# Kernel tuning notes

Hardware: AMD Instinct MI355X
Metric: run time of the kernel (lower is better)

## Reference

```python
import jax, jax.numpy as jnp
import numpy as np


def pool_windows(a, k):
    # a: [..., H, W] with k == stride (non-overlapping windows)
    lead = a.shape[:-2]
    H, W = a.shape[-2], a.shape[-1]
    a = a.reshape(*lead, H // k, k, W // k, k)
    a = jnp.moveaxis(a, -3, -2)            # [..., Ho, Wo, k, k]
    return a.reshape(*lead, H // k, W // k, k * k)


def setup_inputs() -> dict:
    key = jax.random.key(0)
    k1, k2 = jax.random.split(key)
    S, C, H, W = 258, 64, 64, 64
    x = jax.random.normal(k1, (S, C, H, W), dtype=jnp.float32)
    # noise layer (last row) is nonnegative by convention
    x = x.at[-1].set(jnp.abs(x[-1]))
    x_true = jax.random.normal(k2, (C, H, W), dtype=jnp.float32)
    return {"x": x, "x_true": x_true, "kernel_size": 2, "stride": 2}


def reference(x, x_true, kernel_size, stride):
    # Zonotope/interval abstract transformer for MaxPool2d.
    # x: [S, C, H, W]; row 0 = center, rows 1:-1 = eps coeffs, row -1 = noise.
    assert kernel_size == stride
    k = kernel_size

    # Interval bounds per element (sum-of-abs reduction over symbol layers)
    eps_abs = jnp.sum(jnp.abs(x[1:]), axis=0)           # [C, H, W]
    lo = x[0] - eps_abs
    hi = x[0] + eps_abs

    xw = pool_windows(x, k)                              # [S, C, Ho, Wo, K]
    lw = pool_windows(lo, k)                             # [C, Ho, Wo, K]
    uw = pool_windows(hi, k)
    K = xw.shape[-1]

    # Candidate: window element with the largest lower bound
    i_star = jnp.argmax(lw, axis=-1)                     # [C, Ho, Wo]
    l_star = jnp.take_along_axis(lw, i_star[..., None], axis=-1)[..., 0]
    u_max = jnp.max(uw, axis=-1)

    # Max upper bound among the other window elements
    oh = jnp.arange(K) == i_star[..., None]              # one-hot of i_star
    u_other = jnp.max(jnp.where(oh, -jnp.inf, uw), axis=-1)

    # Exact case: the candidate dominates every other element -> pass its
    # affine form through. Otherwise fall back to the sound interval box
    # [l_star, u_max] (center +/- half-width in the noise layer).
    exact = l_star >= u_other                            # [C, Ho, Wo]

    gathered = jnp.take_along_axis(
        xw, i_star[None, ..., None], axis=-1)[..., 0]    # [S, C, Ho, Wo]

    box_center = 0.5 * (l_star + u_max)
    box_noise = 0.5 * (u_max - l_star)

    out_center = jnp.where(exact, gathered[0], box_center)
    out_eps = jnp.where(exact[None], gathered[1:-1], 0.0)
    out_noise = jnp.where(exact, jnp.abs(gathered[-1]), box_noise)

    x_out = jnp.concatenate(
        [out_center[None], out_eps, out_noise[None]], axis=0)

    out_abs = jnp.sum(jnp.abs(x_out[1:]), axis=0)
    x_min = x_out[0] - out_abs
    x_max = x_out[0] + out_abs

    x_true_out = jnp.max(pool_windows(x_true, k), axis=-1)
    return x_out, x_min, x_max, x_true_out
```

## Files before the change

kernel.cpp:

```cpp
#include <hip/hip_runtime.h>
#include <math.h>

#define S    258
#define C    64
#define H    64
#define W    64
#define NP   65536
#define L    262144
#define XOUT (S * NP)
#define NSC  8
#define NQ   4

__global__ __launch_bounds__(256) void k_partial(const float* __restrict__ x,
                                                 float* __restrict__ part,
                                                 float* __restrict__ out) {
    const int b  = blockIdx.x;
    const int sc = b >> 8;
    const int c  = (b >> 2) & 63;
    const int q  = b & 3;
    const int t  = threadIdx.x;

    {
        float4 z = make_float4(0.f, 0.f, 0.f, 0.f);
        float4* zp = (float4*)(out + NP) + (size_t)b * 2048 + t;
        #pragma unroll
        for (int i = 0; i < 8; ++i) zp[i * 256] = z;
    }

    const int s0 = 1 + ((257 * sc) >> 3);
    const int s1 = 1 + ((257 * (sc + 1)) >> 3);

    const int base = c * (H * W) + q * 1024 + 4 * t;
    const float* px = x + (size_t)s0 * L + base;
    float4 acc = make_float4(0.f, 0.f, 0.f, 0.f);
    #pragma unroll 4
    for (int s = s0; s < s1; ++s) {
        float4 v = *(const float4*)px;
        acc.x += fabsf(v.x); acc.y += fabsf(v.y);
        acc.z += fabsf(v.z); acc.w += fabsf(v.w);
        px += L;
    }
    *(float4*)(part + (size_t)sc * L + c * (H * W) + q * 1024 + 4 * t) = acc;
}

__global__ __launch_bounds__(256) void k_decide(const float* __restrict__ x,
                                                const float* __restrict__ x_true,
                                                const float* __restrict__ part,
                                                float* __restrict__ out) {
    __shared__ int ex_n;
    __shared__ int ex_p[256];
    __shared__ int ex_pos[256];

    const int b = blockIdx.x;
    const int c = b >> 2;
    const int q = b & 3;
    const int t = threadIdx.x;
    if (t == 0) ex_n = 0;
    __syncthreads();

    const int r  = t >> 5;
    const int wo = t & 31;
    const int qbase   = c * (H * W) + q * 1024;
    const int loc_top = (2 * r) * W + 2 * wo;
    const int loc_bot = loc_top + W;

    float e0 = 0.f, e1 = 0.f, e2 = 0.f, e3 = 0.f;
    #pragma unroll
    for (int sc = 0; sc < NSC; ++sc) {
        const float* pp = part + (size_t)sc * L + qbase;
        float2 a = *(const float2*)(pp + loc_top);
        float2 d = *(const float2*)(pp + loc_bot);
        e0 += a.x; e1 += a.y; e2 += d.x; e3 += d.y;
    }

    float2 r0 = *(const float2*)(x + qbase + loc_top);
    float2 r1 = *(const float2*)(x + qbase + loc_bot);
    float x0[4]  = { r0.x, r0.y, r1.x, r1.y };
    float eps[4] = { e0, e1, e2, e3 };
    float lo[4], hi[4];
    #pragma unroll
    for (int e = 0; e < 4; ++e) { lo[e] = x0[e] - eps[e]; hi[e] = x0[e] + eps[e]; }

    int istar = 0;
    #pragma unroll
    for (int e = 1; e < 4; ++e) if (lo[e] > lo[istar]) istar = e;

    const float lstar = lo[istar];
    const float umax  = fmaxf(fmaxf(hi[0], hi[1]), fmaxf(hi[2], hi[3]));
    float uoth = -INFINITY;
    #pragma unroll
    for (int e = 0; e < 4; ++e) if (e != istar) uoth = fmaxf(uoth, hi[e]);

    const bool exact = (lstar >= uoth);
    const int  pos   = qbase + loc_top + (istar & 1) + (istar >> 1) * W;

    float center, noise;
    if (exact) {
        center = x0[istar];
        noise  = fabsf(x[(size_t)(S - 1) * L + pos]);
        int i  = atomicAdd(&ex_n, 1);
        ex_p[i]   = c * 1024 + q * 256 + t;
        ex_pos[i] = pos;
    } else {
        center = 0.5f * (lstar + umax);
        noise  = 0.5f * (umax - lstar);
    }

    const int p = c * 1024 + q * 256 + t;
    out[p] = center;
    out[(size_t)(S - 1) * NP + p] = noise;
    out[XOUT + p] = lstar;
    out[XOUT + NP + p] = umax;

    float2 t0 = *(const float2*)(x_true + qbase + loc_top);
    float2 t1 = *(const float2*)(x_true + qbase + loc_bot);
    out[XOUT + 2 * NP + p] = fmaxf(fmaxf(t0.x, t0.y), fmaxf(t1.x, t1.y));

    __syncthreads();
    const int n = ex_n;
    for (int j = 0; j < n; ++j) {
        out[(size_t)(1 + t) * NP + ex_p[j]] = x[(size_t)(1 + t) * L + ex_pos[j]];
    }
}

extern "C" void kernel_launch(void* const* d_in, const int* in_sizes, int n_in,
                              void* d_out, int out_size, void* d_ws, size_t ws_size,
                              hipStream_t stream) {
    const float* x      = (const float*)d_in[0];
    const float* x_true = (const float*)d_in[1];
    float* out  = (float*)d_out;
    float* part = (float*)d_ws;

    k_partial<<<NSC * C * NQ, 256, 0, stream>>>(x, part, out);
    k_decide<<<C * NQ, 256, 0, stream>>>(x, x_true, part, out);
}
```

Before: 383.5 us.

## Fuse partial abs-sum and window decision into a single kernel

```diff
diff --git a/kernel.cpp b/kernel.cpp
--- a/kernel.cpp
+++ b/kernel.cpp
@@ -3,118 +3,107 @@
 
 #define S    258
 #define C    64
-#define H    64
-#define W    64
+#define L    262144
 #define NP   65536
-#define L    262144
 #define XOUT (S * NP)
-#define NSC  8
-#define NQ   4
 
-__global__ __launch_bounds__(256) void k_partial(const float* __restrict__ x,
-                                                 float* __restrict__ part,
-                                                 float* __restrict__ out) {
+__global__ __launch_bounds__(256) void k_fused(const float* __restrict__ x,
+                                               const float* __restrict__ x_true,
+                                               float* __restrict__ out) {
+    __shared__ int ex_n;
+    __shared__ int ex_p[128];
+    __shared__ int ex_pos[128];
+
     const int b  = blockIdx.x;
-    const int sc = b >> 8;
-    const int c  = (b >> 2) & 63;
-    const int q  = b & 3;
+    const int c  = b >> 3;
+    const int hq = b & 7;
     const int t  = threadIdx.x;
+    if (t == 0) ex_n = 0;
 
     {
-        float4 z = make_float4(0.f, 0.f, 0.f, 0.f);
-        float4* zp = (float4*)(out + NP) + (size_t)b * 2048 + t;
+        const float4 z = make_float4(0.f, 0.f, 0.f, 0.f);
+        float4* o4 = (float4*)out + (size_t)(c * 256 + hq * 32 + (t & 31));
+        const int s0 = 1 + (t >> 5);
         #pragma unroll
-        for (int i = 0; i < 8; ++i) zp[i * 256] = z;
+        for (int i = 0; i < 32; ++i)
+            o4[(size_t)(s0 + i * 8) * 16384] = z;
     }
 
-    const int s0 = 1 + ((257 * sc) >> 3);
-    const int s1 = 1 + ((257 * (sc + 1)) >> 3);
+    const int slice = c * 4096 + hq * 512;
+    const float* px = x + slice + 2 * t;
 
-    const int base = c * (H * W) + q * 1024 + 4 * t;
-    const float* px = x + (size_t)s0 * L + base;
-    float4 acc = make_float4(0.f, 0.f, 0.f, 0.f);
-    #pragma unroll 4
-    for (int s = s0; s < s1; ++s) {
-        float4 v = *(const float4*)px;
-        acc.x += fabsf(v.x); acc.y += fabsf(v.y);
-        acc.z += fabsf(v.z); acc.w += fabsf(v.w);
-        px += L;
+    const float2 x0 = *(const float2*)px;
+    float e0 = 0.f, e1 = 0.f;
+    const float* ps = px + L;
+    #pragma unroll 8
+    for (int s = 1; s <= 256; ++s) {
+        float2 v = *(const float2*)ps;
+        e0 += fabsf(v.x);
+        e1 += fabsf(v.y);
+        ps += L;
     }
-    *(float4*)(part + (size_t)sc * L + c * (H * W) + q * 1024 + 4 * t) = acc;
-}
+    const float2 nz = *(const float2*)ps;
+    const float n0 = fabsf(nz.x), n1 = fabsf(nz.y);
+    e0 += n0;
+    e1 += n1;
 
-__global__ __launch_bounds__(256) void k_decide(const float* __restrict__ x,
-                                                const float* __restrict__ x_true,
-                                                const float* __restrict__ part,
-                                                float* __restrict__ out) {
-    __shared__ int ex_n;
-    __shared__ int ex_p[256];
-    __shared__ int ex_pos[256];
-
-    const int b = blockIdx.x;
-    const int c = b >> 2;
-    const int q = b & 3;
-    const int t = threadIdx.x;
-    if (t == 0) ex_n = 0;
     __syncthreads();
 
-    const int r  = t >> 5;
-    const int wo = t & 31;
-    const int qbase   = c * (H * W) + q * 1024;
-    const int loc_top = (2 * r) * W + 2 * wo;
-    const int loc_bot = loc_top + W;
+    const float ox0 = __shfl_xor(x0.x, 32, 64);
+    const float ox1 = __shfl_xor(x0.y, 32, 64);
+    const float oe0 = __shfl_xor(e0,   32, 64);
+    const float oe1 = __shfl_xor(e1,   32, 64);
+    const float on0 = __shfl_xor(n0,   32, 64);
+    const float on1 = __shfl_xor(n1,   32, 64);
 
-    float e0 = 0.f, e1 = 0.f, e2 = 0.f, e3 = 0.f;
-    #pragma unroll
-    for (int sc = 0; sc < NSC; ++sc) {
-        const float* pp = part + (size_t)sc * L + qbase;
-        float2 a = *(const float2*)(pp + loc_top);
-        float2 d = *(const float2*)(pp + loc_bot);
-        e0 += a.x; e1 += a.y; e2 += d.x; e3 += d.y;
+    const int lane = t & 63;
+    if (lane < 32) {
+        const float xc[4] = { x0.x, x0.y, ox0, ox1 };
+        const float ee[4] = { e0,   e1,   oe0, oe1 };
+        const float nn[4] = { n0,   n1,   on0, on1 };
+        float lo[4], hi[4];
+        #pragma unroll
+        for (int e = 0; e < 4; ++e) {
+            lo[e] = xc[e] - ee[e];
+            hi[e] = xc[e] + ee[e];
+        }
+
+        int istar = 0;
+        #pragma unroll
+        for (int e = 1; e < 4; ++e) if (lo[e] > lo[istar]) istar = e;
+
+        const float lstar = lo[istar];
+        const float umax  = fmaxf(fmaxf(hi[0], hi[1]), fmaxf(hi[2], hi[3]));
+        float uoth = -INFINITY;
+        #pragma unroll
+        for (int e = 0; e < 4; ++e) if (e != istar) uoth = fmaxf(uoth, hi[e]);
+
+        const bool exact = (lstar >= uoth);
+        const int  wr    = t >> 6;
+        const int  top   = wr * 128 + lane * 2;
+        const int  pw    = c * 1024 + hq * 128 + wr * 32 + lane;
+
+        float center, noise;
+        if (exact) {
+            center = xc[istar];
+            noise  = nn[istar];
+            const int i = atomicAdd(&ex_n, 1);
+            ex_p[i]   = pw;
+            ex_pos[i] = slice + top + (istar & 1) + (istar >> 1) * 64;
+        } else {
+            center = 0.5f * (lstar + umax);
+            noise  = 0.5f * (umax - lstar);
+        }
+
+        out[pw] = center;
+        out[(size_t)(S - 1) * NP + pw] = noise;
+        out[XOUT + pw] = lstar;
+        out[XOUT + NP + pw] = umax;
+
+        const float2 ta = *(const float2*)(x_true + slice + top);
+        const float2 tb = *(const float2*)(x_true + slice + top + 64);
+        out[XOUT + 2 * NP + pw] = fmaxf(fmaxf(ta.x, ta.y), fmaxf(tb.x, tb.y));
     }
-
-    float2 r0 = *(const float2*)(x + qbase + loc_top);
-    float2 r1 = *(const float2*)(x + qbase + loc_bot);
-    float x0[4]  = { r0.x, r0.y, r1.x, r1.y };
-    float eps[4] = { e0, e1, e2, e3 };
-    float lo[4], hi[4];
-    #pragma unroll
-    for (int e = 0; e < 4; ++e) { lo[e] = x0[e] - eps[e]; hi[e] = x0[e] + eps[e]; }
-
-    int istar = 0;
-    #pragma unroll
-    for (int e = 1; e < 4; ++e) if (lo[e] > lo[istar]) istar = e;
-
-    const float lstar = lo[istar];
-    const float umax  = fmaxf(fmaxf(hi[0], hi[1]), fmaxf(hi[2], hi[3]));
-    float uoth = -INFINITY;
-    #pragma unroll
-    for (int e = 0; e < 4; ++e) if (e != istar) uoth = fmaxf(uoth, hi[e]);
-
-    const bool exact = (lstar >= uoth);
-    const int  pos   = qbase + loc_top + (istar & 1) + (istar >> 1) * W;
-
-    float center, noise;
-    if (exact) {
-        center = x0[istar];
-        noise  = fabsf(x[(size_t)(S - 1) * L + pos]);
-        int i  = atomicAdd(&ex_n, 1);
-        ex_p[i]   = c * 1024 + q * 256 + t;
-        ex_pos[i] = pos;
-    } else {
-        center = 0.5f * (lstar + umax);
-        noise  = 0.5f * (umax - lstar);
-    }
-
-    const int p = c * 1024 + q * 256 + t;
-    out[p] = center;
-    out[(size_t)(S - 1) * NP + p] = noise;
-    out[XOUT + p] = lstar;
-    out[XOUT + NP + p] = umax;
-
-    float2 t0 = *(const float2*)(x_true + qbase + loc_top);
-    float2 t1 = *(const float2*)(x_true + qbase + loc_bot);
-    out[XOUT + 2 * NP + p] = fmaxf(fmaxf(t0.x, t0.y), fmaxf(t1.x, t1.y));
 
     __syncthreads();
     const int n = ex_n;
@@ -128,9 +117,5 @@
                               hipStream_t stream) {
     const float* x      = (const float*)d_in[0];
     const float* x_true = (const float*)d_in[1];
-    float* out  = (float*)d_out;
-    float* part = (float*)d_ws;
-
-    k_partial<<<NSC * C * NQ, 256, 0, stream>>>(x, part, out);
-    k_decide<<<C * NQ, 256, 0, stream>>>(x, x_true, part, out);
+    k_fused<<<C * 8, 256, 0, stream>>>(x, x_true, (float*)d_out);
 }
```

After: 383.8 us. Within noise of the previous version (+0.1%).
